# Performance work log

Hardware: AMD Instinct MI355X
Metric: run time of the kernel (lower is better)

Reference implementation:

```python
import jax, jax.numpy as jnp
from jax import lax
import numpy as np

FEAT_STRIDE = 16
RATIOS = np.array([0.5, 1.0, 2.0])
SCALES = np.array([8.0, 16.0, 32.0])
PRE_NMS = 6000
POST_NMS = 300
NMS_THRESH = 0.7
MIN_SIZE = 16.0
A = 9  # num anchors per location


def _whctrs(a):
    w = a[2] - a[0] + 1.0
    h = a[3] - a[1] + 1.0
    return w, h, a[0] + 0.5 * (w - 1.0), a[1] + 0.5 * (h - 1.0)


def _mkanchors(ws, hs, cx, cy):
    return np.stack([cx - 0.5 * (ws - 1.0), cy - 0.5 * (hs - 1.0),
                     cx + 0.5 * (ws - 1.0), cy + 0.5 * (hs - 1.0)], axis=1)


def generate_anchors(base_size=16):
    base = np.array([1.0, 1.0, base_size, base_size]) - 1.0
    w, h, cx, cy = _whctrs(base)
    size = w * h
    ws = np.round(np.sqrt(size / RATIOS))
    hs = np.round(ws * RATIOS)
    ratio_anchors = _mkanchors(ws, hs, cx, cy)
    out = []
    for ra in ratio_anchors:
        w, h, cx, cy = _whctrs(ra)
        out.append(_mkanchors(w * SCALES, h * SCALES, cx, cy))
    return np.concatenate(out, axis=0).astype(np.float32)  # [9,4]


def setup_inputs() -> dict:
    key = jax.random.key(0)
    k1, k2 = jax.random.split(key)
    scores = jax.random.normal(k1, (1, 2 * A, 50, 80), dtype=jnp.float32)
    bbox_deltas = jax.random.normal(k2, (1, 4 * A, 50, 80), dtype=jnp.float32) * 0.5
    im_info = jnp.array([[800.0, 1280.0, 1.5]], dtype=jnp.float32)  # (h, w, scale)
    return {"scores": scores, "bbox_deltas": bbox_deltas, "im_info": im_info}


def reference(scores, bbox_deltas, im_info):
    base_anchors = jnp.asarray(generate_anchors())  # [A,4]
    H, W = scores.shape[-2], scores.shape[-1]

    # fg scores, flattened in (h, w, a) order to match anchor ordering
    sc = scores[:, A:, :, :].transpose(0, 2, 3, 1).reshape(-1)  # [K*A]

    # anchors for every feature-map location
    sx = (jnp.arange(W) * FEAT_STRIDE).astype(jnp.float32)
    sy = (jnp.arange(H) * FEAT_STRIDE).astype(jnp.float32)
    gy, gx = jnp.meshgrid(sy, sx, indexing="ij")
    shifts = jnp.stack([gx, gy, gx, gy], axis=-1).reshape(-1, 1, 4)  # [K,1,4]
    anchors = (base_anchors[None, :, :] + shifts).reshape(-1, 4)    # [K*A,4]

    # decode deltas (dw/dh clamped to [-10,10])
    d = bbox_deltas.transpose(0, 2, 3, 1).reshape(-1, 4)
    d = jnp.concatenate([d[:, :2], jnp.clip(d[:, 2:], -10.0, 10.0)], axis=1)
    aw = anchors[:, 2] - anchors[:, 0] + 1.0
    ah = anchors[:, 3] - anchors[:, 1] + 1.0
    acx = anchors[:, 0] + 0.5 * aw
    acy = anchors[:, 1] + 0.5 * ah
    pcx = d[:, 0] * aw + acx
    pcy = d[:, 1] * ah + acy
    pw = jnp.exp(d[:, 2]) * aw
    ph = jnp.exp(d[:, 3]) * ah
    boxes = jnp.stack([pcx - 0.5 * pw, pcy - 0.5 * ph,
                       pcx + 0.5 * pw, pcy + 0.5 * ph], axis=1)

    # clip to image
    im_h, im_w, im_s = im_info[0, 0], im_info[0, 1], im_info[0, 2]
    boxes = jnp.stack([
        jnp.clip(boxes[:, 0], 0.0, im_w - 1.0),
        jnp.clip(boxes[:, 1], 0.0, im_h - 1.0),
        jnp.clip(boxes[:, 2], 0.0, im_w - 1.0),
        jnp.clip(boxes[:, 3], 0.0, im_h - 1.0),
    ], axis=1)

    # min-size filter (masking instead of compaction, for static shapes)
    ws = boxes[:, 2] - boxes[:, 0] + 1.0
    hs = boxes[:, 3] - boxes[:, 1] + 1.0
    min_sz = MIN_SIZE * im_s
    valid = (ws >= min_sz) & (hs >= min_sz)
    sc = jnp.where(valid, sc, -jnp.inf)

    # pre-NMS top-k by score
    top_sc, top_idx = lax.top_k(sc, PRE_NMS)
    props = boxes[top_idx]  # [P,4], sorted by descending score
    alive0 = jnp.isfinite(top_sc)

    # pairwise IoU (the +1 pixel convention matching the rest of the pipeline)
    x1, y1, x2, y2 = props[:, 0], props[:, 1], props[:, 2], props[:, 3]
    areas = (x2 - x1 + 1.0) * (y2 - y1 + 1.0)
    iw = jnp.clip(jnp.minimum(x2[:, None], x2[None, :]) - jnp.maximum(x1[:, None], x1[None, :]) + 1.0, 0.0)
    ih = jnp.clip(jnp.minimum(y2[:, None], y2[None, :]) - jnp.maximum(y1[:, None], y1[None, :]) + 1.0, 0.0)
    inter = iw * ih
    iou = inter / (areas[:, None] + areas[None, :] - inter)  # [P,P] ~144MB

    idx = jnp.arange(PRE_NMS)

    def body(i, keep):
        sup = keep[i] & (iou[i] > NMS_THRESH) & (idx > i)
        return keep & ~sup

    keep = lax.fori_loop(0, PRE_NMS, body, alive0)

    # gather first POST_NMS kept proposals into fixed-size output [POST_NMS,5]
    rank = jnp.cumsum(keep) - 1
    dest = jnp.where(keep & (rank < POST_NMS), rank, POST_NMS)
    out = jnp.zeros((POST_NMS + 1, 5), dtype=scores.dtype)
    out = out.at[dest, 1:].set(props)
    return out[:POST_NMS]
```

## Files before the change

### kernel.cpp

```cpp
#include <hip/hip_runtime.h>
#include <stdint.h>

#define A_NUM 9
#define H_FM 50
#define W_FM 80
#define HW (H_FM * W_FM)
#define N_ANCH (A_NUM * HW)
#define PRE_NMS_N 6000
#define POST_NMS_N 300
#define NMS_TH 0.7f
#define MASK_W 94
#define MASK_STRIDE 96
#define NBIN 4096
#define BIN_CAP 4096
#define NBD 141
#define TILE_J 1024
#define JT 6
#define MTILES (JT * MASK_W)

typedef unsigned long long ull;

__constant__ float c_aw[9] = {184.f,368.f,736.f,128.f,256.f,512.f, 88.f,176.f,352.f};
__constant__ float c_ah[9] = { 96.f,192.f,384.f,128.f,256.f,512.f,176.f,352.f,704.f};

__device__ int    g_hist[NBIN];
__device__ ull    g_dead[MASK_STRIDE];
__device__ ull    g_rowany[MASK_STRIDE];
__device__ float4 g_boxes[N_ANCH];
__device__ float4 g_props[PRE_NMS_N];
__device__ ull    g_mask[(size_t)PRE_NMS_N * MASK_STRIDE];
__device__ ull    g_colsup[MASK_W * 64];

__device__ __forceinline__ float iou_of(float4 bi, float ai, float4 bj, float aj) {
    float iw = fminf(bi.z, bj.z) - fmaxf(bi.x, bj.x) + 1.f;
    float ih = fminf(bi.w, bj.w) - fmaxf(bi.y, bj.y) + 1.f;
    iw = fmaxf(iw, 0.f);
    ih = fmaxf(ih, 0.f);
    float inter = iw * ih;
    return inter / (ai + aj - inter);
}

__global__ __launch_bounds__(256) void k_decode(const float* __restrict__ scores,
                                                const float* __restrict__ deltas,
                                                const float* __restrict__ iminfo,
                                                ull* __restrict__ bins) {
    int t = blockIdx.x * 256 + threadIdx.x;
    if (t >= N_ANCH) return;
    int a    = t / HW;
    int cell = t - a * HW;
    int x    = cell % W_FM;
    int y    = cell / W_FM;

    float sc = scores[(A_NUM + a) * HW + cell];

    int dbase = (a * 4) * HW + cell;
    float d0 = deltas[dbase];
    float d1 = deltas[dbase + HW];
    float d2 = deltas[dbase + 2 * HW];
    float d3 = deltas[dbase + 3 * HW];
    d2 = fminf(fmaxf(d2, -10.f), 10.f);
    d3 = fminf(fmaxf(d3, -10.f), 10.f);

    float aw = c_aw[a], ah = c_ah[a];
    float acx = (float)(x * 16 + 8);
    float acy = (float)(y * 16 + 8);

    float pcx = d0 * aw + acx;
    float pcy = d1 * ah + acy;
    float pw  = expf(d2) * aw;
    float ph  = expf(d3) * ah;

    float x1 = pcx - 0.5f * pw;
    float y1 = pcy - 0.5f * ph;
    float x2 = pcx + 0.5f * pw;
    float y2 = pcy + 0.5f * ph;

    float imh = iminfo[0], imw = iminfo[1], ims = iminfo[2];
    x1 = fminf(fmaxf(x1, 0.f), imw - 1.f);
    y1 = fminf(fmaxf(y1, 0.f), imh - 1.f);
    x2 = fminf(fmaxf(x2, 0.f), imw - 1.f);
    y2 = fminf(fmaxf(y2, 0.f), imh - 1.f);

    float wsz = x2 - x1 + 1.f;
    float hsz = y2 - y1 + 1.f;
    float minsz = 16.f * ims;
    bool valid = (wsz >= minsz) && (hsz >= minsz);

    g_boxes[t] = make_float4(x1, y1, x2, y2);

    unsigned int u   = __float_as_uint(sc);
    unsigned int asc = (u & 0x80000000u) ? ~u : (u | 0x80000000u);
    unsigned int dk  = ~asc;
    if (!valid) dk = 0xFF800000u;

    unsigned int ikey = (unsigned int)(cell * A_NUM + a);
    ull key = ((ull)dk << 32) | ikey;

    int bin  = (int)(dk >> 20);
    int slot = atomicAdd(&g_hist[bin], 1);
    if (slot < BIN_CAP) bins[(size_t)bin * BIN_CAP + slot] = key;
}

__global__ __launch_bounds__(256) void k_binsort(const ull* __restrict__ bins) {
    __shared__ ull sb[4096];
    __shared__ int red[256];
    int b = blockIdx.x;
    int cntf = g_hist[b];
    if (cntf == 0) return;
    int tid = threadIdx.x;

    int part = 0;
    for (int j = tid; j < b; j += 256) part += g_hist[j];
    red[tid] = part;
    __syncthreads();
    for (int off = 128; off > 0; off >>= 1) {
        if (tid < off) red[tid] += red[tid + off];
        __syncthreads();
    }
    int s0 = red[0];
    if (s0 >= PRE_NMS_N) return;

    int cnt = (cntf < BIN_CAP) ? cntf : BIN_CAP;
    const ull* seg = bins + (size_t)b * BIN_CAP;

    int P = 2; while (P < cnt) P <<= 1;
    for (int i = tid; i < P; i += 256) sb[i] = (i < cnt) ? seg[i] : ~0ULL;
    __syncthreads();
    for (int k2 = 2; k2 <= P; k2 <<= 1) {
        for (int j = k2 >> 1; j >= 1; j >>= 1) {
            for (int p = tid; p < (P >> 1); p += 256) {
                int i  = ((p & ~(j - 1)) << 1) | (p & (j - 1));
                int pr = i | j;
                bool up = ((i & k2) == 0);
                ull a = sb[i], c = sb[pr];
                if ((a > c) == up) { sb[i] = c; sb[pr] = a; }
            }
            __syncthreads();
        }
    }
    for (int i = tid; i < cnt; i += 256) {
        int r = s0 + i;
        if (r < PRE_NMS_N) {
            ull key = sb[i];
            unsigned int dk = (unsigned int)(key >> 32);
            if (dk < 0xFF800000u) {
                unsigned int ik = (unsigned int)key;
                int tt = (int)(ik % A_NUM) * HW + (int)(ik / A_NUM);
                g_props[r] = g_boxes[tt];
            } else {
                g_props[r] = make_float4(0.f, 0.f, 0.f, 0.f);
                atomicOr(&g_dead[r >> 6], 1ULL << (r & 63));
            }
        }
    }
}

__global__ __launch_bounds__(256) void k_maskcol() {
    __shared__ float4 sj[16 * 65];
    __shared__ float  sa[16 * 65];
    __shared__ ull    s_row;
    int vb = blockIdx.x;
    int tid = threadIdx.x;

    if (vb < 16) g_hist[vb * 256 + tid] = 0;

    if (vb < MTILES) {
        int by = vb / JT;
        int bx = vb % JT;

        if (bx * TILE_J + (TILE_J - 1) <= by * 64) return;

        if (tid == 0) s_row = 0ULL;

        int jbase = bx * TILE_J;
        for (int c = tid; c < TILE_J; c += 256) {
            int jj = jbase + c;
            float4 bjs = (jj < PRE_NMS_N) ? g_props[jj] : make_float4(0.f, 0.f, 0.f, 0.f);
            int q = c >> 6, r = c & 63;
            sj[q * 65 + r] = bjs;
            sa[q * 65 + r] = (bjs.z - bjs.x + 1.f) * (bjs.w - bjs.y + 1.f);
        }
        __syncthreads();

        ull rowbits = 0;
        for (int c = tid; c < 1024; c += 256) {
            int li = c >> 4;
            int wl = c & 15;
            int i  = by * 64 + li;
            int w  = bx * 16 + wl;
            if (i >= PRE_NMS_N || w >= MASK_W) continue;

            float4 bi = g_props[i];
            float ai = (bi.z - bi.x + 1.f) * (bi.w - bi.y + 1.f);
            int jstart = w * 64;
            int bstart = i + 1 - jstart; if (bstart < 0) bstart = 0;
            int bend = PRE_NMS_N - jstart; if (bend > 64) bend = 64;
            const float4* sw = &sj[wl * 65];
            const float*  swa = &sa[wl * 65];
            ull bits = 0;
            for (int b = bstart; b < bend; ++b) {
                if (iou_of(bi, ai, sw[b], swa[b]) > NMS_TH) bits |= (1ULL << b);
            }
            g_mask[(size_t)i * MASK_STRIDE + w] = bits;
            if (bits && w != (i >> 6)) rowbits |= (1ULL << (i & 63));
        }
        if (rowbits) atomicOr(&s_row, rowbits);
        __syncthreads();
        if (tid == 0 && s_row) atomicOr(&g_rowany[by], s_row);
    } else {
        int w = vb - MTILES;
        int gj = w * 64 + tid;
        if (tid < 64)
            sj[tid] = (gj < PRE_NMS_N) ? g_props[gj] : make_float4(0.f, 0.f, 0.f, 0.f);
        __syncthreads();
        if (tid < 64) {
            float4 bj = sj[tid];
            float aj = (bj.z - bj.x + 1.f) * (bj.w - bj.y + 1.f);
            ull bits = 0;
            for (int b = 0; b < tid; ++b) {
                float4 bi = sj[b];
                float ai = (bi.z - bi.x + 1.f) * (bi.w - bi.y + 1.f);
                if (iou_of(bi, ai, bj, aj) > NMS_TH) bits |= (1ULL << b);
            }
            g_colsup[gj] = bits;
        }
    }
}

#define BATCH 8
__global__ __launch_bounds__(256, 1) void k_scan(float* __restrict__ out) {
    __shared__ ull scol[MASK_W * 64];
    __shared__ ull srow[MASK_W];
    __shared__ int s_kept[POST_NMS_N];
    __shared__ int s_kc;
    int tid = threadIdx.x;

    for (int i = tid; i < MASK_W * 64; i += 256) scol[i] = g_colsup[i];
    for (int i = tid; i < MASK_W; i += 256)      srow[i] = g_rowany[i];
    __syncthreads();

    if (tid < 64) {
        int lane = tid;
        ull rm0 = g_dead[lane];
        ull rm1 = (lane < MASK_W - 64) ? g_dead[64 + lane] : ~0ULL;
        if (lane == 29) rm1 |= 0xFFFF000000000000ULL;
        int kc = 0;
        int pw = -2;
        ull dnext = 0;

        for (;;) {
            ull avail0 = __ballot(~rm0 != 0ULL);
            ull avail1 = __ballot(~rm1 != 0ULL);
            int w;
            if (avail0)      w = __ffsll(avail0) - 1;
            else if (avail1) w = 63 + __ffsll(avail1);
            else break;

            ull diag = (w == pw + 1) ? dnext : scol[(w << 6) + lane];
            if (w + 1 < MASK_W) dnext = scol[((w + 1) << 6) + lane];
            pw = w;

            ull raw = srow[w];
            ull rmw = (w < 64) ? rm0 : rm1;
            int ri  = (w < 64) ? w : w - 64;
            unsigned clo = __builtin_amdgcn_readlane((unsigned)rmw, ri);
            unsigned chi = __builtin_amdgcn_readlane((unsigned)(rmw >> 32), ri);
            ull curw = ((ull)chi << 32) | clo;

            ull U = ~curw;
            ull K = 0;
            while (U) {
                ull UK = U | K;
                bool deadp = (diag & K)  != 0ULL;
                bool freep = (diag & UK) == 0ULL;
                ull nd = __ballot(deadp) & U;
                U &= ~nd;
                ull nk = __ballot(freep) & U;
                U &= ~nk;
                K |= nk;
                if (!nk && !nd) break;
            }

            int cnt  = __popcll(K);
            int take = min(cnt, POST_NMS_N - kc);
            if (K & (1ULL << lane)) {
                int pos = kc + __popcll(K & ((1ULL << lane) - 1ULL));
                if (pos < POST_NMS_N) s_kept[pos] = (w << 6) + lane;
            }
            kc += take;
            if (kc >= POST_NMS_N) break;

            if (w < 64) { if (lane == w)      rm0 = ~0ULL; }
            else        { if (lane == w - 64) rm1 = ~0ULL; }

            ull need = K & raw;
            while (need) {
                int id[BATCH];
                int n = 0;
#pragma unroll
                for (int t2 = 0; t2 < BATCH; ++t2) {
                    id[t2] = 0;
                    if (need) { id[t2] = __ffsll(need) - 1; need &= need - 1; n = t2 + 1; }
                }
                ull v0[BATCH], v1[BATCH];
#pragma unroll
                for (int t2 = 0; t2 < BATCH; ++t2) {
                    const ull* __restrict__ row =
                        g_mask + (size_t)((w << 6) + id[t2]) * MASK_STRIDE;
                    v0[t2] = row[lane];
                    v1[t2] = (lane < MASK_W - 64) ? row[64 + lane] : 0ULL;
                }
                ull a0 = 0, a1 = 0;
#pragma unroll
                for (int t2 = 0; t2 < BATCH; ++t2) {
                    ull m = (t2 < n) ? ~0ULL : 0ULL;
                    a0 |= v0[t2] & m;
                    a1 |= v1[t2] & m;
                }
                rm0 |= a0;
                rm1 |= a1;
            }
        }
        if (lane == 0) s_kc = (kc < POST_NMS_N) ? kc : POST_NMS_N;
    }
    __syncthreads();

    for (int i = tid; i < MASK_STRIDE; i += 256) {
        g_dead[i] = 0ULL;
        g_rowany[i] = 0ULL;
    }

    int kcf = s_kc;
    for (int r = tid; r < POST_NMS_N; r += 256) {
        float4 p = make_float4(0.f, 0.f, 0.f, 0.f);
        if (r < kcf) p = g_props[s_kept[r]];
        out[r * 5 + 0] = 0.f;
        out[r * 5 + 1] = p.x;
        out[r * 5 + 2] = p.y;
        out[r * 5 + 3] = p.z;
        out[r * 5 + 4] = p.w;
    }
}

extern "C" void kernel_launch(void* const* d_in, const int* in_sizes, int n_in,
                              void* d_out, int out_size, void* d_ws, size_t ws_size,
                              hipStream_t stream) {
    const float* scores = (const float*)d_in[0];
    const float* deltas = (const float*)d_in[1];
    const float* iminfo = (const float*)d_in[2];
    float* out = (float*)d_out;
    ull* bins = (ull*)d_ws;

    k_decode<<<NBD, 256, 0, stream>>>(scores, deltas, iminfo, bins);
    k_binsort<<<NBIN, 256, 0, stream>>>(bins);
    k_maskcol<<<MTILES + MASK_W, 256, 0, stream>>>();
    k_scan<<<1, 256, 0, stream>>>(out);
}
```

Baseline: 124.5 us.

## Replace IoU division with cross-multiplied compare and compute two mask rows per thread

```diff
diff --git a/kernel.cpp b/kernel.cpp
--- a/kernel.cpp
+++ b/kernel.cpp
@@ -14,9 +14,8 @@
 #define NBIN 4096
 #define BIN_CAP 4096
 #define NBD 141
-#define TILE_J 1024
-#define JT 6
-#define MTILES (JT * MASK_W)
+#define JT 12
+#define MTILES (94 * JT)
 
 typedef unsigned long long ull;
 
@@ -31,13 +30,13 @@
 __device__ ull    g_mask[(size_t)PRE_NMS_N * MASK_STRIDE];
 __device__ ull    g_colsup[MASK_W * 64];
 
-__device__ __forceinline__ float iou_of(float4 bi, float ai, float4 bj, float aj) {
+__device__ __forceinline__ bool sup_of(float4 bi, float ai, float4 bj, float aj) {
     float iw = fminf(bi.z, bj.z) - fmaxf(bi.x, bj.x) + 1.f;
     float ih = fminf(bi.w, bj.w) - fmaxf(bi.y, bj.y) + 1.f;
     iw = fmaxf(iw, 0.f);
     ih = fmaxf(ih, 0.f);
     float inter = iw * ih;
-    return inter / (ai + aj - inter);
+    return 1.7f * inter > 0.7f * (ai + aj);
 }
 
 __global__ __launch_bounds__(256) void k_decode(const float* __restrict__ scores,
@@ -156,8 +155,8 @@
 }
 
 __global__ __launch_bounds__(256) void k_maskcol() {
-    __shared__ float4 sj[16 * 65];
-    __shared__ float  sa[16 * 65];
+    __shared__ float4 sj[8 * 65];
+    __shared__ float  sa[8 * 65];
     __shared__ ull    s_row;
     int vb = blockIdx.x;
     int tid = threadIdx.x;
@@ -168,12 +167,12 @@
         int by = vb / JT;
         int bx = vb % JT;
 
-        if (bx * TILE_J + (TILE_J - 1) <= by * 64) return;
+        if (bx * 512 + 511 <= by * 64) return;
 
         if (tid == 0) s_row = 0ULL;
 
-        int jbase = bx * TILE_J;
-        for (int c = tid; c < TILE_J; c += 256) {
+        int jbase = bx * 512;
+        for (int c = tid; c < 512; c += 256) {
             int jj = jbase + c;
             float4 bjs = (jj < PRE_NMS_N) ? g_props[jj] : make_float4(0.f, 0.f, 0.f, 0.f);
             int q = c >> 6, r = c & 63;
@@ -182,27 +181,50 @@
         }
         __syncthreads();
 
+        int wl = tid & 7;
+        int rp = tid >> 3;
+        int i0 = by * 64 + rp * 2;
+        int i1 = i0 + 1;
+        int w  = bx * 8 + wl;
+
         ull rowbits = 0;
-        for (int c = tid; c < 1024; c += 256) {
-            int li = c >> 4;
-            int wl = c & 15;
-            int i  = by * 64 + li;
-            int w  = bx * 16 + wl;
-            if (i >= PRE_NMS_N || w >= MASK_W) continue;
-
-            float4 bi = g_props[i];
-            float ai = (bi.z - bi.x + 1.f) * (bi.w - bi.y + 1.f);
+        if (w < MASK_W) {
+            bool act0 = (i0 < PRE_NMS_N);
+            bool act1 = (i1 < PRE_NMS_N);
+            float4 bi0 = act0 ? g_props[i0] : make_float4(0.f, 0.f, 0.f, 0.f);
+            float4 bi1 = act1 ? g_props[i1] : make_float4(0.f, 0.f, 0.f, 0.f);
+            float a0 = (bi0.z - bi0.x + 1.f) * (bi0.w - bi0.y + 1.f);
+            float a1 = (bi1.z - bi1.x + 1.f) * (bi1.w - bi1.y + 1.f);
+
             int jstart = w * 64;
-            int bstart = i + 1 - jstart; if (bstart < 0) bstart = 0;
-            int bend = PRE_NMS_N - jstart; if (bend > 64) bend = 64;
-            const float4* sw = &sj[wl * 65];
+            int bs = i0 + 1 - jstart; if (bs < 0) bs = 0;
+            int be = PRE_NMS_N - jstart; if (be > 64) be = 64;
+            const float4* sw  = &sj[wl * 65];
             const float*  swa = &sa[wl * 65];
-            ull bits = 0;
-            for (int b = bstart; b < bend; ++b) {
-                if (iou_of(bi, ai, sw[b], swa[b]) > NMS_TH) bits |= (1ULL << b);
-            }
-            g_mask[(size_t)i * MASK_STRIDE + w] = bits;
-            if (bits && w != (i >> 6)) rowbits |= (1ULL << (i & 63));
+            ull bits0 = 0, bits1 = 0;
+            for (int b = bs; b < be; ++b) {
+                float4 bj = sw[b];
+                float aj = swa[b];
+                float iw0 = fminf(bi0.z, bj.z) - fmaxf(bi0.x, bj.x) + 1.f;
+                float ih0 = fminf(bi0.w, bj.w) - fmaxf(bi0.y, bj.y) + 1.f;
+                float in0 = fmaxf(iw0, 0.f) * fmaxf(ih0, 0.f);
+                float iw1 = fminf(bi1.z, bj.z) - fmaxf(bi1.x, bj.x) + 1.f;
+                float ih1 = fminf(bi1.w, bj.w) - fmaxf(bi1.y, bj.y) + 1.f;
+                float in1 = fmaxf(iw1, 0.f) * fmaxf(ih1, 0.f);
+                if (1.7f * in0 > 0.7f * (a0 + aj)) bits0 |= (1ULL << b);
+                if (1.7f * in1 > 0.7f * (a1 + aj)) bits1 |= (1ULL << b);
+            }
+            int bself = i1 - jstart;
+            if (bself >= 0 && bself < 64) bits1 &= ~(1ULL << bself);
+
+            if (act0) {
+                g_mask[(size_t)i0 * MASK_STRIDE + w] = bits0;
+                if (bits0 && w != (i0 >> 6)) rowbits |= (1ULL << (i0 & 63));
+            }
+            if (act1) {
+                g_mask[(size_t)i1 * MASK_STRIDE + w] = bits1;
+                if (bits1 && w != (i1 >> 6)) rowbits |= (1ULL << (i1 & 63));
+            }
         }
         if (rowbits) atomicOr(&s_row, rowbits);
         __syncthreads();
@@ -220,7 +242,7 @@
             for (int b = 0; b < tid; ++b) {
                 float4 bi = sj[b];
                 float ai = (bi.z - bi.x + 1.f) * (bi.w - bi.y + 1.f);
-                if (iou_of(bi, ai, bj, aj) > NMS_TH) bits |= (1ULL << b);
+                if (sup_of(bi, ai, bj, aj)) bits |= (1ULL << b);
             }
             g_colsup[gj] = bits;
         }
```

After: 106.0 us (median of 2 runs). 1.17x faster.
